# Kernel optimization log

Hardware: AMD Instinct MI355X
Metric: run time of the kernel (lower is better)

Reference implementation:

```python
import jax, jax.numpy as jnp
import numpy as np

N_NODES = 100000
N_EDGES = 1600000
F_IN = 128
HID = 128
N_CLS = 7


def _sage_conv(x, src, dst, Wl, bl, Wr, n_nodes, deg_inv):
    # mean-aggregate neighbor messages at destination nodes
    msg = x[src]                                            # [E, d] gather
    agg = jax.ops.segment_sum(msg, dst, num_segments=n_nodes)
    agg = agg * deg_inv[:, None]                            # mean
    # PyG SAGEConv: lin_l(aggr) + lin_r(x); bias only on lin_l
    return agg @ Wl.T + bl + x @ Wr.T


def setup_inputs() -> dict:
    key = jax.random.key(0)
    ks = jax.random.split(key, 12)
    x = jax.random.normal(ks[0], (N_NODES, F_IN), dtype=jnp.float32)
    edge_index = jax.random.randint(ks[1], (2, N_EDGES), 0, N_NODES, dtype=jnp.int32)
    s = 0.05
    return {
        "x": x,
        "edge_index": edge_index,
        "W1l": jax.random.normal(ks[2], (HID, F_IN), dtype=jnp.float32) * s,
        "b1": jax.random.normal(ks[3], (HID,), dtype=jnp.float32) * s,
        "W1r": jax.random.normal(ks[4], (HID, F_IN), dtype=jnp.float32) * s,
        "W2l": jax.random.normal(ks[5], (HID, HID), dtype=jnp.float32) * s,
        "b2": jax.random.normal(ks[6], (HID,), dtype=jnp.float32) * s,
        "W2r": jax.random.normal(ks[7], (HID, HID), dtype=jnp.float32) * s,
        "W3l": jax.random.normal(ks[8], (N_CLS, HID), dtype=jnp.float32) * s,
        "b3": jax.random.normal(ks[9], (N_CLS,), dtype=jnp.float32) * s,
        "W3r": jax.random.normal(ks[10], (N_CLS, HID), dtype=jnp.float32) * s,
    }


def reference(x, edge_index, W1l, b1, W1r, W2l, b2, W2r, W3l, b3, W3r):
    src, dst = edge_index[0], edge_index[1]
    n = x.shape[0]
    # in-degree for mean aggregation (shared by all layers)
    deg = jax.ops.segment_sum(jnp.ones((src.shape[0],), x.dtype), dst, num_segments=n)
    deg_inv = jnp.where(deg > 0, 1.0 / deg, 0.0)

    h = _sage_conv(x, src, dst, W1l, b1, W1r, n, deg_inv)
    h = jax.nn.relu(h)  # dropout is identity in eval mode
    h = _sage_conv(h, src, dst, W2l, b2, W2r, n, deg_inv)
    h = jax.nn.relu(h)
    h = _sage_conv(h, src, dst, W3l, b3, W3r, n, deg_inv)
    return jax.nn.log_softmax(h, axis=1)
```

## Files before the change

kernel.cpp:

```cpp
#include <hip/hip_runtime.h>
#include <hip/hip_bf16.h>

#define NFEAT 128

typedef __attribute__((ext_vector_type(8))) short frag8;
typedef __attribute__((ext_vector_type(4))) float f32x4;

__device__ __forceinline__ unsigned short f2bf(float f) {
  unsigned int u = __builtin_bit_cast(unsigned int, f);
  u += 0x7fffu + ((u >> 16) & 1u);
  return (unsigned short)(u >> 16);
}
__device__ __forceinline__ float bf2f(unsigned short s) {
  return __builtin_bit_cast(float, ((unsigned int)s) << 16);
}
__device__ __forceinline__ unsigned int pack2(float lo, float hi) {
  return (unsigned int)f2bf(lo) | ((unsigned int)f2bf(hi) << 16);
}

__global__ __launch_bounds__(256) void k_bucket_count(
    const int* __restrict__ dst, int* __restrict__ bucket_cnt, int E, int NB, int chunk) {
  __shared__ int hist[512];
  int t = threadIdx.x;
  hist[t] = 0;
  hist[t + 256] = 0;
  __syncthreads();
  int beg = blockIdx.x * chunk, end = min(beg + chunk, E);
  for (int i = beg + t; i < end; i += 256) atomicAdd(&hist[dst[i] >> 8], 1);
  __syncthreads();
  for (int k = t; k < NB; k += 256)
    if (hist[k]) atomicAdd(&bucket_cnt[k], hist[k]);
}

__global__ void k_bucket_scan(const int* __restrict__ bucket_cnt,
                              int* __restrict__ bucket_base,
                              int* __restrict__ bucket_cursor, int NB, int E) {
  __shared__ int sm[512];
  int t = threadIdx.x;
  int v = (t < NB) ? bucket_cnt[t] : 0;
  sm[t] = v;
  __syncthreads();
  for (int off = 1; off < 512; off <<= 1) {
    int add = (t >= off) ? sm[t - off] : 0;
    __syncthreads();
    sm[t] += add;
    __syncthreads();
  }
  int excl = sm[t] - v;
  if (t < NB) {
    bucket_base[t] = excl;
    bucket_cursor[t] = excl;
  }
  if (t == 0) bucket_base[NB] = E;
}

__global__ __launch_bounds__(256) void k_bucket_fill(
    const int* __restrict__ src, const int* __restrict__ dst,
    int* __restrict__ bucket_cursor, unsigned int* __restrict__ tmp,
    int E, int NB, int chunk) {
  __shared__ int hist[512];
  __shared__ int cur[512];
  int t = threadIdx.x;
  hist[t] = 0;
  hist[t + 256] = 0;
  __syncthreads();
  int beg = blockIdx.x * chunk, end = min(beg + chunk, E);
  for (int i = beg + t; i < end; i += 256) atomicAdd(&hist[dst[i] >> 8], 1);
  __syncthreads();
  for (int k = t; k < 512; k += 256)
    cur[k] = (k < NB && hist[k]) ? atomicAdd(&bucket_cursor[k], hist[k]) : 0;
  __syncthreads();
  for (int i = beg + t; i < end; i += 256) {
    int d = dst[i];
    int p = atomicAdd(&cur[d >> 8], 1);
    tmp[p] = (((unsigned int)(d & 255)) << 24) | (unsigned int)src[i];
  }
}

__global__ __launch_bounds__(256) void k_local_sort(
    const unsigned int* __restrict__ tmp, const int* __restrict__ bucket_base,
    int* __restrict__ csr, int* __restrict__ row_ptr, float* __restrict__ dinv,
    int N, int E) {
  __shared__ int cnt[256];
  __shared__ int scan_s[256];
  int b = blockIdx.x, t = threadIdx.x;
  int base = bucket_base[b];
  int cnt_b = bucket_base[b + 1] - base;
  cnt[t] = 0;
  __syncthreads();
  for (int i = t; i < cnt_b; i += 256) atomicAdd(&cnt[tmp[base + i] >> 24], 1);
  __syncthreads();
  int v = cnt[t];
  scan_s[t] = v;
  __syncthreads();
  for (int off = 1; off < 256; off <<= 1) {
    int add = (t >= off) ? scan_s[t - off] : 0;
    __syncthreads();
    scan_s[t] += add;
    __syncthreads();
  }
  int excl = scan_s[t] - v;
  int node = b * 256 + t;
  if (node <= N) row_ptr[node] = base + excl;
  if (node < N) dinv[node] = (v > 0) ? (1.0f / (float)v) : 0.0f;
  __syncthreads();
  cnt[t] = base + excl;
  __syncthreads();
  for (int i = t; i < cnt_b; i += 256) {
    unsigned int u = tmp[base + i];
    int q = atomicAdd(&cnt[u >> 24], 1);
    csr[q] = (int)(u & 0x00FFFFFFu);
  }
}

__global__ void k_cvtw(const float* __restrict__ w0, const float* __restrict__ w1,
                       const float* __restrict__ w2, const float* __restrict__ w3,
                       unsigned short* __restrict__ out) {
  int i = blockIdx.x * blockDim.x + threadIdx.x;
  int m = i >> 14, off = i & 16383;
  const float* src = (m == 0) ? w0 : (m == 1) ? w1 : (m == 2) ? w2 : w3;
  out[i] = f2bf(src[off]);
}

__global__ void k_cvtx(const float* __restrict__ x, unsigned int* __restrict__ out,
                       int n_pairs) {
  int i = blockIdx.x * blockDim.x + threadIdx.x;
  if (i < n_pairs) {
    float2 v = *(const float2*)(x + (size_t)i * 2);
    out[i] = pack2(v.x, v.y);
  }
}

template <bool IN_F32>
__global__ __launch_bounds__(256) void k_aggregate(
    const void* __restrict__ Xin, const int* __restrict__ row_ptr,
    const int* __restrict__ csr, const float* __restrict__ dinv,
    unsigned int* __restrict__ Aout, int n) {
  int wv = threadIdx.x >> 6, lane = threadIdx.x & 63;
  int v = blockIdx.x * 4 + wv;
  if (v >= n) return;
  int beg = row_ptr[v], end = row_ptr[v + 1];
  float dv = dinv[v];

  if constexpr (IN_F32) {
    const float* xp = (const float*)Xin;
    int slot = lane >> 5;
    int part = lane & 31;
    float acc[4] = {0.f, 0.f, 0.f, 0.f};
    for (int j = beg; j < end; j += 16) {
      float4 f[8];
#pragma unroll
      for (int b = 0; b < 8; ++b) {
        f[b] = make_float4(0.f, 0.f, 0.f, 0.f);
        int e = j + b * 2 + slot;
        if (e < end) {
          int si = csr[e];
          f[b] = *(const float4*)(xp + (size_t)si * NFEAT + part * 4);
        }
      }
#pragma unroll
      for (int b = 0; b < 8; ++b) {
        acc[0] += f[b].x; acc[1] += f[b].y; acc[2] += f[b].z; acc[3] += f[b].w;
      }
    }
#pragma unroll
    for (int k = 0; k < 4; ++k) acc[k] += __shfl_xor(acc[k], 32);
    if (slot == 0) {
      uint2 o;
      o.x = pack2(acc[0] * dv, acc[1] * dv);
      o.y = pack2(acc[2] * dv, acc[3] * dv);
      *(uint2*)(Aout + (size_t)v * (NFEAT / 2) + part * 2) = o;
    }
  } else {
    const unsigned int* xp = (const unsigned int*)Xin;
    int slot = lane >> 4;
    int part = lane & 15;
    float acc[8] = {0.f, 0.f, 0.f, 0.f, 0.f, 0.f, 0.f, 0.f};
    for (int j = beg; j < end; j += 16) {
      uint4 f[4];
#pragma unroll
      for (int b = 0; b < 4; ++b) {
        f[b] = make_uint4(0u, 0u, 0u, 0u);
        int e = j + b * 4 + slot;
        if (e < end) {
          int si = csr[e];
          f[b] = *(const uint4*)(xp + (size_t)si * (NFEAT / 2) + part * 4);
        }
      }
#pragma unroll
      for (int b = 0; b < 4; ++b) {
        acc[0] += bf2f((unsigned short)(f[b].x & 0xffffu));
        acc[1] += bf2f((unsigned short)(f[b].x >> 16));
        acc[2] += bf2f((unsigned short)(f[b].y & 0xffffu));
        acc[3] += bf2f((unsigned short)(f[b].y >> 16));
        acc[4] += bf2f((unsigned short)(f[b].z & 0xffffu));
        acc[5] += bf2f((unsigned short)(f[b].z >> 16));
        acc[6] += bf2f((unsigned short)(f[b].w & 0xffffu));
        acc[7] += bf2f((unsigned short)(f[b].w >> 16));
      }
    }
#pragma unroll
    for (int k = 0; k < 8; ++k) {
      acc[k] += __shfl_xor(acc[k], 16);
      acc[k] += __shfl_xor(acc[k], 32);
    }
    if (slot == 0) {
      uint4 o;
      o.x = pack2(acc[0] * dv, acc[1] * dv);
      o.y = pack2(acc[2] * dv, acc[3] * dv);
      o.z = pack2(acc[4] * dv, acc[5] * dv);
      o.w = pack2(acc[6] * dv, acc[7] * dv);
      *(uint4*)(Aout + (size_t)v * (NFEAT / 2) + part * 4) = o;
    }
  }
}

template <bool X_IS_F32>
__global__ __launch_bounds__(256, 4) void k_gemm(
    const unsigned short* __restrict__ A, const void* __restrict__ X,
    const unsigned short* __restrict__ Wl, const unsigned short* __restrict__ Wr,
    const float* __restrict__ bias, unsigned short* __restrict__ Out,
    int M, int ntiles) {
  int wv = threadIdx.x >> 6, lane = threadIdx.x & 63;
  int lr = lane & 15, kq = lane >> 4;
  int kb0 = kq * 8;

  frag8 wl[2][4], wr[2][4];
  float bias_c[2];
#pragma unroll
  for (int ci = 0; ci < 2; ++ci) {
    int wrow = (wv * 2 + ci) * 16 + lr;
    bias_c[ci] = bias[wrow];
#pragma unroll
    for (int kk = 0; kk < 4; ++kk) {
      wl[ci][kk] = *(const frag8*)(Wl + (size_t)wrow * NFEAT + kk * 32 + kb0);
      wr[ci][kk] = *(const frag8*)(Wr + (size_t)wrow * NFEAT + kk * 32 + kb0);
    }
  }

  for (int tile = blockIdx.x; tile < ntiles; tile += gridDim.x) {
    int m0 = tile * 16;
    int row = m0 + lr;
    bool rowok = row < M;
    frag8 aA[4], aX[4];
#pragma unroll
    for (int kk = 0; kk < 4; ++kk) {
      aA[kk] = frag8{};
      aX[kk] = frag8{};
      if (rowok) {
        aA[kk] = *(const frag8*)(A + (size_t)row * NFEAT + kk * 32 + kb0);
        if constexpr (X_IS_F32) {
          const float* xp = (const float*)X + (size_t)row * NFEAT + kk * 32 + kb0;
          float4 v0 = *(const float4*)xp;
          float4 v1 = *(const float4*)(xp + 4);
          frag8 a;
          a[0] = (short)f2bf(v0.x); a[1] = (short)f2bf(v0.y);
          a[2] = (short)f2bf(v0.z); a[3] = (short)f2bf(v0.w);
          a[4] = (short)f2bf(v1.x); a[5] = (short)f2bf(v1.y);
          a[6] = (short)f2bf(v1.z); a[7] = (short)f2bf(v1.w);
          aX[kk] = a;
        } else {
          aX[kk] = *(const frag8*)((const unsigned short*)X + (size_t)row * NFEAT + kk * 32 + kb0);
        }
      }
    }
    __syncthreads();
    f32x4 acc[2] = {};
#pragma unroll
    for (int kk = 0; kk < 4; ++kk) {
#pragma unroll
      for (int ci = 0; ci < 2; ++ci) {
        acc[ci] = __builtin_amdgcn_mfma_f32_16x16x32_bf16(aA[kk], wl[ci][kk], acc[ci], 0, 0, 0);
        acc[ci] = __builtin_amdgcn_mfma_f32_16x16x32_bf16(aX[kk], wr[ci][kk], acc[ci], 0, 0, 0);
      }
    }
#pragma unroll
    for (int ci = 0; ci < 2; ++ci) {
#pragma unroll
      for (int r = 0; r < 4; ++r) {
        int orow = m0 + kq * 4 + r;
        if (orow < M) {
          int ocol = (wv * 2 + ci) * 16 + lr;
          float val = acc[ci][r] + bias_c[ci];
          Out[(size_t)orow * NFEAT + ocol] = f2bf(fmaxf(val, 0.f));
        }
      }
    }
  }
}

__global__ void k_layer3(const unsigned int* __restrict__ A,
                         const unsigned int* __restrict__ H,
                         const float* __restrict__ W3l, const float* __restrict__ b3,
                         const float* __restrict__ W3r, float* __restrict__ out, int n) {
  int wv = threadIdx.x >> 6, lane = threadIdx.x & 63;
  int v = blockIdx.x * 4 + wv;
  if (v >= n) return;
  unsigned int ua = A[(size_t)v * (NFEAT / 2) + lane];
  unsigned int uh = H[(size_t)v * (NFEAT / 2) + lane];
  float a0 = bf2f((unsigned short)(ua & 0xffffu)), a1 = bf2f((unsigned short)(ua >> 16));
  float h0 = bf2f((unsigned short)(uh & 0xffffu)), h1 = bf2f((unsigned short)(uh >> 16));
  float s[7];
#pragma unroll
  for (int c = 0; c < 7; ++c) {
    float2 wl = *(const float2*)(W3l + c * NFEAT + lane * 2);
    float2 wr = *(const float2*)(W3r + c * NFEAT + lane * 2);
    s[c] = a0 * wl.x + a1 * wl.y + h0 * wr.x + h1 * wr.y;
  }
#pragma unroll
  for (int off = 32; off > 0; off >>= 1) {
#pragma unroll
    for (int c = 0; c < 7; ++c) s[c] += __shfl_xor(s[c], off);
  }
  float z[7], mx = -1e30f;
#pragma unroll
  for (int c = 0; c < 7; ++c) {
    z[c] = s[c] + b3[c];
    mx = fmaxf(mx, z[c]);
  }
  float se = 0.f;
#pragma unroll
  for (int c = 0; c < 7; ++c) se += __expf(z[c] - mx);
  float lse = mx + __logf(se);
  float val = z[0];
#pragma unroll
  for (int c = 1; c < 7; ++c) val = (lane == c) ? z[c] : val;
  if (lane < 7) out[(size_t)v * 7 + lane] = val - lse;
}

extern "C" void kernel_launch(void* const* d_in, const int* in_sizes, int n_in,
                              void* d_out, int out_size, void* d_ws, size_t ws_size,
                              hipStream_t stream) {
  const float* x = (const float*)d_in[0];
  const int* ei = (const int*)d_in[1];
  const float* W1l = (const float*)d_in[2];
  const float* b1 = (const float*)d_in[3];
  const float* W1r = (const float*)d_in[4];
  const float* W2l = (const float*)d_in[5];
  const float* b2 = (const float*)d_in[6];
  const float* W2r = (const float*)d_in[7];
  const float* W3l = (const float*)d_in[8];
  const float* b3 = (const float*)d_in[9];
  const float* W3r = (const float*)d_in[10];
  float* out = (float*)d_out;

  int N = in_sizes[0] / NFEAT;
  int E = in_sizes[1] / 2;
  const int* src = ei;
  const int* dst = ei + E;

  char* ws = (char*)d_ws;
  size_t off = 0;
  auto alloc = [&](size_t bytes) {
    void* p = (void*)(ws + off);
    off += (bytes + 255) & ~(size_t)255;
    return p;
  };
  int* row_ptr = (int*)alloc((size_t)(N + 1) * 4);
  float* dinv = (float*)alloc((size_t)N * 4);
  int* bucket_cnt = (int*)alloc(512 * 4);
  int* bucket_base = (int*)alloc(513 * 4);
  int* bucket_cursor = (int*)alloc(512 * 4);
  int* csr = (int*)alloc((size_t)E * 4);
  unsigned short* Wbf = (unsigned short*)alloc((size_t)4 * 128 * 128 * 2);
  unsigned short* Abuf = (unsigned short*)alloc((size_t)N * NFEAT * 2);
  unsigned short* Bbuf = (unsigned short*)alloc((size_t)N * NFEAT * 2);
  size_t off_base = off;
  unsigned short* Xbf = (unsigned short*)alloc((size_t)N * NFEAT * 2);
  bool use_xbf = (off <= ws_size);
  if (!use_xbf) off = off_base;
  unsigned int* tmp = (unsigned int*)Abuf;

  int NB = (N + 255) >> 8;
  int chunk = (E + 255) / 256;

  hipMemsetAsync(bucket_cnt, 0, 512 * 4, stream);
  k_bucket_count<<<256, 256, 0, stream>>>(dst, bucket_cnt, E, NB, chunk);
  k_bucket_scan<<<1, 512, 0, stream>>>(bucket_cnt, bucket_base, bucket_cursor, NB, E);
  k_bucket_fill<<<256, 256, 0, stream>>>(src, dst, bucket_cursor, tmp, E, NB, chunk);
  k_local_sort<<<NB, 256, 0, stream>>>(tmp, bucket_base, csr, row_ptr, dinv, N, E);
  k_cvtw<<<(4 * 128 * 128) / 256, 256, 0, stream>>>(W1l, W1r, W2l, W2r, Wbf);
  if (use_xbf) {
    int npairs = N * (NFEAT / 2);
    k_cvtx<<<(npairs + 255) / 256, 256, 0, stream>>>(x, (unsigned int*)Xbf, npairs);
  }

  unsigned short* W1l_bf = Wbf;
  unsigned short* W1r_bf = Wbf + 16384;
  unsigned short* W2l_bf = Wbf + 32768;
  unsigned short* W2r_bf = Wbf + 49152;

  int gagg = (N + 3) / 4;
  int ntiles = (N + 15) / 16;
  int ggemm = min(ntiles, 1024);

  if (use_xbf) {
    k_aggregate<false><<<gagg, 256, 0, stream>>>(Xbf, row_ptr, csr, dinv,
                                                 (unsigned int*)Abuf, N);
    k_gemm<false><<<ggemm, 256, 0, stream>>>(Abuf, Xbf, W1l_bf, W1r_bf, b1, Bbuf, N, ntiles);
  } else {
    k_aggregate<true><<<gagg, 256, 0, stream>>>(x, row_ptr, csr, dinv,
                                                (unsigned int*)Abuf, N);
    k_gemm<true><<<ggemm, 256, 0, stream>>>(Abuf, x, W1l_bf, W1r_bf, b1, Bbuf, N, ntiles);
  }
  k_aggregate<false><<<gagg, 256, 0, stream>>>(Bbuf, row_ptr, csr, dinv,
                                               (unsigned int*)Abuf, N);
  k_gemm<false><<<ggemm, 256, 0, stream>>>(Abuf, Bbuf, W2l_bf, W2r_bf, b2, Bbuf, N, ntiles);
  k_aggregate<false><<<gagg, 256, 0, stream>>>(Bbuf, row_ptr, csr, dinv,
                                               (unsigned int*)Abuf, N);
  k_layer3<<<gagg, 256, 0, stream>>>((const unsigned int*)Abuf, (const unsigned int*)Bbuf,
                                     W3l, b3, W3r, out, N);
}
```

Baseline: 375.4 us.

## Process two nodes per wavefront in aggregation and fuse layer-3 aggregate with head

```diff
diff --git a/kernel.cpp b/kernel.cpp
--- a/kernel.cpp
+++ b/kernel.cpp
@@ -16,6 +16,16 @@
 }
 __device__ __forceinline__ unsigned int pack2(float lo, float hi) {
   return (unsigned int)f2bf(lo) | ((unsigned int)f2bf(hi) << 16);
+}
+__device__ __forceinline__ void acc_pair(float* acc, unsigned int u) {
+  acc[0] += __builtin_bit_cast(float, u << 16);
+  acc[1] += __builtin_bit_cast(float, u & 0xffff0000u);
+}
+__device__ __forceinline__ void acc_uint4(float* a, const uint4& f) {
+  acc_pair(a + 0, f.x);
+  acc_pair(a + 2, f.y);
+  acc_pair(a + 4, f.z);
+  acc_pair(a + 6, f.w);
 }
 
 __global__ __launch_bounds__(256) void k_bucket_count(
@@ -131,9 +141,78 @@
   }
 }
 
-template <bool IN_F32>
-__global__ __launch_bounds__(256) void k_aggregate(
-    const void* __restrict__ Xin, const int* __restrict__ row_ptr,
+__global__ __launch_bounds__(256) void k_aggregate2(
+    const unsigned int* __restrict__ xp, const int* __restrict__ row_ptr,
+    const int* __restrict__ csr, const float* __restrict__ dinv,
+    unsigned int* __restrict__ Aout, int n) {
+  int wv = threadIdx.x >> 6, lane = threadIdx.x & 63;
+  int v0 = (blockIdx.x * 4 + wv) * 2;
+  if (v0 >= n) return;
+  int v1 = v0 + 1;
+  bool has1 = v1 < n;
+  int beg0 = row_ptr[v0], end0 = row_ptr[v0 + 1];
+  int beg1 = end0;
+  int end1 = has1 ? row_ptr[v1 + 1] : beg1;
+  int slot = lane >> 4, part = lane & 15;
+
+  float a0[8] = {0.f, 0.f, 0.f, 0.f, 0.f, 0.f, 0.f, 0.f};
+  float a1[8] = {0.f, 0.f, 0.f, 0.f, 0.f, 0.f, 0.f, 0.f};
+  int j0 = beg0, j1 = beg1;
+  while (j0 < end0 || j1 < end1) {
+    uint4 f0[4], f1[4];
+#pragma unroll
+    for (int b = 0; b < 4; ++b) {
+      f0[b] = make_uint4(0u, 0u, 0u, 0u);
+      int e = j0 + b * 4 + slot;
+      if (e < end0) {
+        int s = csr[e];
+        f0[b] = *(const uint4*)(xp + (size_t)s * (NFEAT / 2) + part * 4);
+      }
+    }
+#pragma unroll
+    for (int b = 0; b < 4; ++b) {
+      f1[b] = make_uint4(0u, 0u, 0u, 0u);
+      int e = j1 + b * 4 + slot;
+      if (e < end1) {
+        int s = csr[e];
+        f1[b] = *(const uint4*)(xp + (size_t)s * (NFEAT / 2) + part * 4);
+      }
+    }
+#pragma unroll
+    for (int b = 0; b < 4; ++b) acc_uint4(a0, f0[b]);
+#pragma unroll
+    for (int b = 0; b < 4; ++b) acc_uint4(a1, f1[b]);
+    j0 += 16;
+    j1 += 16;
+  }
+#pragma unroll
+  for (int k = 0; k < 8; ++k) {
+    a0[k] += __shfl_xor(a0[k], 16);
+    a0[k] += __shfl_xor(a0[k], 32);
+    a1[k] += __shfl_xor(a1[k], 16);
+    a1[k] += __shfl_xor(a1[k], 32);
+  }
+  if (slot == 0) {
+    float d0 = dinv[v0];
+    uint4 o;
+    o.x = pack2(a0[0] * d0, a0[1] * d0);
+    o.y = pack2(a0[2] * d0, a0[3] * d0);
+    o.z = pack2(a0[4] * d0, a0[5] * d0);
+    o.w = pack2(a0[6] * d0, a0[7] * d0);
+    *(uint4*)(Aout + (size_t)v0 * (NFEAT / 2) + part * 4) = o;
+  } else if (slot == 1 && has1) {
+    float d1 = dinv[v1];
+    uint4 o;
+    o.x = pack2(a1[0] * d1, a1[1] * d1);
+    o.y = pack2(a1[2] * d1, a1[3] * d1);
+    o.z = pack2(a1[4] * d1, a1[5] * d1);
+    o.w = pack2(a1[6] * d1, a1[7] * d1);
+    *(uint4*)(Aout + (size_t)v1 * (NFEAT / 2) + part * 4) = o;
+  }
+}
+
+__global__ __launch_bounds__(256) void k_aggregate_f32(
+    const float* __restrict__ xp, const int* __restrict__ row_ptr,
     const int* __restrict__ csr, const float* __restrict__ dinv,
     unsigned int* __restrict__ Aout, int n) {
   int wv = threadIdx.x >> 6, lane = threadIdx.x & 63;
@@ -141,77 +220,32 @@
   if (v >= n) return;
   int beg = row_ptr[v], end = row_ptr[v + 1];
   float dv = dinv[v];
-
-  if constexpr (IN_F32) {
-    const float* xp = (const float*)Xin;
-    int slot = lane >> 5;
-    int part = lane & 31;
-    float acc[4] = {0.f, 0.f, 0.f, 0.f};
-    for (int j = beg; j < end; j += 16) {
-      float4 f[8];
-#pragma unroll
-      for (int b = 0; b < 8; ++b) {
-        f[b] = make_float4(0.f, 0.f, 0.f, 0.f);
-        int e = j + b * 2 + slot;
-        if (e < end) {
-          int si = csr[e];
-          f[b] = *(const float4*)(xp + (size_t)si * NFEAT + part * 4);
-        }
-      }
-#pragma unroll
-      for (int b = 0; b < 8; ++b) {
-        acc[0] += f[b].x; acc[1] += f[b].y; acc[2] += f[b].z; acc[3] += f[b].w;
-      }
-    }
-#pragma unroll
-    for (int k = 0; k < 4; ++k) acc[k] += __shfl_xor(acc[k], 32);
-    if (slot == 0) {
-      uint2 o;
-      o.x = pack2(acc[0] * dv, acc[1] * dv);
-      o.y = pack2(acc[2] * dv, acc[3] * dv);
-      *(uint2*)(Aout + (size_t)v * (NFEAT / 2) + part * 2) = o;
-    }
-  } else {
-    const unsigned int* xp = (const unsigned int*)Xin;
-    int slot = lane >> 4;
-    int part = lane & 15;
-    float acc[8] = {0.f, 0.f, 0.f, 0.f, 0.f, 0.f, 0.f, 0.f};
-    for (int j = beg; j < end; j += 16) {
-      uint4 f[4];
-#pragma unroll
-      for (int b = 0; b < 4; ++b) {
-        f[b] = make_uint4(0u, 0u, 0u, 0u);
-        int e = j + b * 4 + slot;
-        if (e < end) {
-          int si = csr[e];
-          f[b] = *(const uint4*)(xp + (size_t)si * (NFEAT / 2) + part * 4);
-        }
-      }
-#pragma unroll
-      for (int b = 0; b < 4; ++b) {
-        acc[0] += bf2f((unsigned short)(f[b].x & 0xffffu));
-        acc[1] += bf2f((unsigned short)(f[b].x >> 16));
-        acc[2] += bf2f((unsigned short)(f[b].y & 0xffffu));
-        acc[3] += bf2f((unsigned short)(f[b].y >> 16));
-        acc[4] += bf2f((unsigned short)(f[b].z & 0xffffu));
-        acc[5] += bf2f((unsigned short)(f[b].z >> 16));
-        acc[6] += bf2f((unsigned short)(f[b].w & 0xffffu));
-        acc[7] += bf2f((unsigned short)(f[b].w >> 16));
-      }
-    }
-#pragma unroll
-    for (int k = 0; k < 8; ++k) {
-      acc[k] += __shfl_xor(acc[k], 16);
-      acc[k] += __shfl_xor(acc[k], 32);
-    }
-    if (slot == 0) {
-      uint4 o;
-      o.x = pack2(acc[0] * dv, acc[1] * dv);
-      o.y = pack2(acc[2] * dv, acc[3] * dv);
-      o.z = pack2(acc[4] * dv, acc[5] * dv);
-      o.w = pack2(acc[6] * dv, acc[7] * dv);
-      *(uint4*)(Aout + (size_t)v * (NFEAT / 2) + part * 4) = o;
-    }
+  int slot = lane >> 5;
+  int part = lane & 31;
+  float acc[4] = {0.f, 0.f, 0.f, 0.f};
+  for (int j = beg; j < end; j += 16) {
+    float4 f[8];
+#pragma unroll
+    for (int b = 0; b < 8; ++b) {
+      f[b] = make_float4(0.f, 0.f, 0.f, 0.f);
+      int e = j + b * 2 + slot;
+      if (e < end) {
+        int si = csr[e];
+        f[b] = *(const float4*)(xp + (size_t)si * NFEAT + part * 4);
+      }
+    }
+#pragma unroll
+    for (int b = 0; b < 8; ++b) {
+      acc[0] += f[b].x; acc[1] += f[b].y; acc[2] += f[b].z; acc[3] += f[b].w;
+    }
+  }
+#pragma unroll
+  for (int k = 0; k < 4; ++k) acc[k] += __shfl_xor(acc[k], 32);
+  if (slot == 0) {
+    uint2 o;
+    o.x = pack2(acc[0] * dv, acc[1] * dv);
+    o.y = pack2(acc[2] * dv, acc[3] * dv);
+    *(uint2*)(Aout + (size_t)v * (NFEAT / 2) + part * 2) = o;
   }
 }
 
@@ -289,43 +323,127 @@
   }
 }
 
-__global__ void k_layer3(const unsigned int* __restrict__ A,
-                         const unsigned int* __restrict__ H,
-                         const float* __restrict__ W3l, const float* __restrict__ b3,
-                         const float* __restrict__ W3r, float* __restrict__ out, int n) {
+__global__ __launch_bounds__(256) void k_layer3f(
+    const unsigned int* __restrict__ H, const int* __restrict__ row_ptr,
+    const int* __restrict__ csr, const float* __restrict__ dinv,
+    const float* __restrict__ W3l, const float* __restrict__ b3,
+    const float* __restrict__ W3r, float* __restrict__ out, int n) {
   int wv = threadIdx.x >> 6, lane = threadIdx.x & 63;
-  int v = blockIdx.x * 4 + wv;
-  if (v >= n) return;
-  unsigned int ua = A[(size_t)v * (NFEAT / 2) + lane];
-  unsigned int uh = H[(size_t)v * (NFEAT / 2) + lane];
-  float a0 = bf2f((unsigned short)(ua & 0xffffu)), a1 = bf2f((unsigned short)(ua >> 16));
-  float h0 = bf2f((unsigned short)(uh & 0xffffu)), h1 = bf2f((unsigned short)(uh >> 16));
-  float s[7];
+  int v0 = (blockIdx.x * 4 + wv) * 2;
+  if (v0 >= n) return;
+  int v1 = v0 + 1;
+  bool has1 = v1 < n;
+  int beg0 = row_ptr[v0], end0 = row_ptr[v0 + 1];
+  int beg1 = end0;
+  int end1 = has1 ? row_ptr[v1 + 1] : beg1;
+  int slot = lane >> 4, part = lane & 15;
+
+  float a0[8] = {0.f, 0.f, 0.f, 0.f, 0.f, 0.f, 0.f, 0.f};
+  float a1[8] = {0.f, 0.f, 0.f, 0.f, 0.f, 0.f, 0.f, 0.f};
+  int j0 = beg0, j1 = beg1;
+  while (j0 < end0 || j1 < end1) {
+    uint4 f0[4], f1[4];
+#pragma unroll
+    for (int b = 0; b < 4; ++b) {
+      f0[b] = make_uint4(0u, 0u, 0u, 0u);
+      int e = j0 + b * 4 + slot;
+      if (e < end0) {
+        int s = csr[e];
+        f0[b] = *(const uint4*)(H + (size_t)s * (NFEAT / 2) + part * 4);
+      }
+    }
+#pragma unroll
+    for (int b = 0; b < 4; ++b) {
+      f1[b] = make_uint4(0u, 0u, 0u, 0u);
+      int e = j1 + b * 4 + slot;
+      if (e < end1) {
+        int s = csr[e];
+        f1[b] = *(const uint4*)(H + (size_t)s * (NFEAT / 2) + part * 4);
+      }
+    }
+#pragma unroll
+    for (int b = 0; b < 4; ++b) acc_uint4(a0, f0[b]);
+#pragma unroll
+    for (int b = 0; b < 4; ++b) acc_uint4(a1, f1[b]);
+    j0 += 16;
+    j1 += 16;
+  }
+#pragma unroll
+  for (int k = 0; k < 8; ++k) {
+    a0[k] += __shfl_xor(a0[k], 16);
+    a0[k] += __shfl_xor(a0[k], 32);
+    a1[k] += __shfl_xor(a1[k], 16);
+    a1[k] += __shfl_xor(a1[k], 32);
+  }
+  float d0 = dinv[v0], d1 = has1 ? dinv[v1] : 0.f;
+#pragma unroll
+  for (int k = 0; k < 8; ++k) {
+    a0[k] *= d0;
+    a1[k] *= d1;
+  }
+  uint4 hu0 = *(const uint4*)(H + (size_t)v0 * (NFEAT / 2) + part * 4);
+  uint4 hu1 = has1 ? *(const uint4*)(H + (size_t)v1 * (NFEAT / 2) + part * 4)
+                   : make_uint4(0u, 0u, 0u, 0u);
+  float h0[8], h1[8];
+  h0[0] = bf2f((unsigned short)(hu0.x & 0xffffu)); h0[1] = bf2f((unsigned short)(hu0.x >> 16));
+  h0[2] = bf2f((unsigned short)(hu0.y & 0xffffu)); h0[3] = bf2f((unsigned short)(hu0.y >> 16));
+  h0[4] = bf2f((unsigned short)(hu0.z & 0xffffu)); h0[5] = bf2f((unsigned short)(hu0.z >> 16));
+  h0[6] = bf2f((unsigned short)(hu0.w & 0xffffu)); h0[7] = bf2f((unsigned short)(hu0.w >> 16));
+  h1[0] = bf2f((unsigned short)(hu1.x & 0xffffu)); h1[1] = bf2f((unsigned short)(hu1.x >> 16));
+  h1[2] = bf2f((unsigned short)(hu1.y & 0xffffu)); h1[3] = bf2f((unsigned short)(hu1.y >> 16));
+  h1[4] = bf2f((unsigned short)(hu1.z & 0xffffu)); h1[5] = bf2f((unsigned short)(hu1.z >> 16));
+  h1[6] = bf2f((unsigned short)(hu1.w & 0xffffu)); h1[7] = bf2f((unsigned short)(hu1.w >> 16));
+
+  float s0[7], s1[7];
 #pragma unroll
   for (int c = 0; c < 7; ++c) {
-    float2 wl = *(const float2*)(W3l + c * NFEAT + lane * 2);
-    float2 wr = *(const float2*)(W3r + c * NFEAT + lane * 2);
-    s[c] = a0 * wl.x + a1 * wl.y + h0 * wr.x + h1 * wr.y;
-  }
-#pragma unroll
-  for (int off = 32; off > 0; off >>= 1) {
-#pragma unroll
-    for (int c = 0; c < 7; ++c) s[c] += __shfl_xor(s[c], off);
-  }
-  float z[7], mx = -1e30f;
+    const float* wlp = W3l + c * NFEAT + part * 8;
+    const float* wrp = W3r + c * NFEAT + part * 8;
+    float4 wl0 = *(const float4*)wlp, wl1 = *(const float4*)(wlp + 4);
+    float4 wr0 = *(const float4*)wrp, wr1 = *(const float4*)(wrp + 4);
+    float t0 = a0[0] * wl0.x + a0[1] * wl0.y + a0[2] * wl0.z + a0[3] * wl0.w +
+               a0[4] * wl1.x + a0[5] * wl1.y + a0[6] * wl1.z + a0[7] * wl1.w +
+               h0[0] * wr0.x + h0[1] * wr0.y + h0[2] * wr0.z + h0[3] * wr0.w +
+               h0[4] * wr1.x + h0[5] * wr1.y + h0[6] * wr1.z + h0[7] * wr1.w;
+    float t1 = a1[0] * wl0.x + a1[1] * wl0.y + a1[2] * wl0.z + a1[3] * wl0.w +
+               a1[4] * wl1.x + a1[5] * wl1.y + a1[6] * wl1.z + a1[7] * wl1.w +
+               h1[0] * wr0.x + h1[1] * wr0.y + h1[2] * wr0.z + h1[3] * wr0.w +
+               h1[4] * wr1.x + h1[5] * wr1.y + h1[6] * wr1.z + h1[7] * wr1.w;
+    s0[c] = t0;
+    s1[c] = t1;
+  }
 #pragma unroll
   for (int c = 0; c < 7; ++c) {
-    z[c] = s[c] + b3[c];
-    mx = fmaxf(mx, z[c]);
-  }
-  float se = 0.f;
-#pragma unroll
-  for (int c = 0; c < 7; ++c) se += __expf(z[c] - mx);
-  float lse = mx + __logf(se);
-  float val = z[0];
-#pragma unroll
-  for (int c = 1; c < 7; ++c) val = (lane == c) ? z[c] : val;
-  if (lane < 7) out[(size_t)v * 7 + lane] = val - lse;
+#pragma unroll
+    for (int off = 1; off < 16; off <<= 1) {
+      s0[c] += __shfl_xor(s0[c], off);
+      s1[c] += __shfl_xor(s1[c], off);
+    }
+  }
+  float z0[7], z1[7], mx0 = -1e30f, mx1 = -1e30f;
+#pragma unroll
+  for (int c = 0; c < 7; ++c) {
+    z0[c] = s0[c] + b3[c];
+    z1[c] = s1[c] + b3[c];
+    mx0 = fmaxf(mx0, z0[c]);
+    mx1 = fmaxf(mx1, z1[c]);
+  }
+  float se0 = 0.f, se1 = 0.f;
+#pragma unroll
+  for (int c = 0; c < 7; ++c) {
+    se0 += __expf(z0[c] - mx0);
+    se1 += __expf(z1[c] - mx1);
+  }
+  float lse0 = mx0 + __logf(se0);
+  float lse1 = mx1 + __logf(se1);
+  float val0 = z0[0], val1 = z1[0];
+#pragma unroll
+  for (int c = 1; c < 7; ++c) {
+    val0 = (part == c) ? z0[c] : val0;
+    val1 = (part == c) ? z1[c] : val1;
+  }
+  if (slot == 0 && part < 7) out[(size_t)v0 * 7 + part] = val0 - lse0;
+  if (slot == 1 && part < 7 && has1) out[(size_t)v1 * 7 + part] = val1 - lse1;
 }
 
 extern "C" void kernel_launch(void* const* d_in, const int* in_sizes, int n_in,
@@ -390,24 +508,23 @@
   unsigned short* W2l_bf = Wbf + 32768;
   unsigned short* W2r_bf = Wbf + 49152;
 
-  int gagg = (N + 3) / 4;
+  int gagg2 = (N + 7) / 8;
   int ntiles = (N + 15) / 16;
   int ggemm = min(ntiles, 1024);
 
   if (use_xbf) {
-    k_aggregate<false><<<gagg, 256, 0, stream>>>(Xbf, row_ptr, csr, dinv,
-                                                 (unsigned int*)Abuf, N);
+    k_aggregate2<<<gagg2, 256, 0, stream>>>((const unsigned int*)Xbf, row_ptr, csr, dinv,
+                                            (unsigned int*)Abuf, N);
     k_gemm<false><<<ggemm, 256, 0, stream>>>(Abuf, Xbf, W1l_bf, W1r_bf, b1, Bbuf, N, ntiles);
   } else {
-    k_aggregate<true><<<gagg, 256, 0, stream>>>(x, row_ptr, csr, dinv,
-                                                (unsigned int*)Abuf, N);
+    int gagg1 = (N + 3) / 4;
+    k_aggregate_f32<<<gagg1, 256, 0, stream>>>(x, row_ptr, csr, dinv,
+                                               (unsigned int*)Abuf, N);
     k_gemm<true><<<ggemm, 256, 0, stream>>>(Abuf, x, W1l_bf, W1r_bf, b1, Bbuf, N, ntiles);
   }
-  k_aggregate<false><<<gagg, 256, 0, stream>>>(Bbuf, row_ptr, csr, dinv,
-                                               (unsigned int*)Abuf, N);
+  k_aggregate2<<<gagg2, 256, 0, stream>>>((const unsigned int*)Bbuf, row_ptr, csr, dinv,
+                                          (unsigned int*)Abuf, N);
   k_gemm<false><<<ggemm, 256, 0, stream>>>(Abuf, Bbuf, W2l_bf, W2r_bf, b2, Bbuf, N, ntiles);
-  k_aggregate<false><<<gagg, 256, 0, stream>>>(Bbuf, row_ptr, csr, dinv,
-                                               (unsigned int*)Abuf, N);
-  k_layer3<<<gagg, 256, 0, stream>>>((const unsigned int*)Abuf, (const unsigned int*)Bbuf,
-                                     W3l, b3, W3r, out, N);
-}
+  k_layer3f<<<gagg2, 256, 0, stream>>>((const unsigned int*)Bbuf, row_ptr, csr, dinv,
+                                       W3l, b3, W3r, out, N);
+}
```

Measured after the change: 412.6 us. 1.1x slower.
